# Optimization experiments

Measured on AMD Instinct MI355X. Metric: run time of the kernel, lower is better.

## Reference

```python
import jax, jax.numpy as jnp
import numpy as np

EMB = 16      # importance embedding channels (ch 0 = logit, 1: = cov features)
NSEG = 196    # n_segments (14x14 superpixel grid)
MC = 16       # num_monte_carlo
TEMP = 1.0    # initial Gumbel/RelaxedBernoulli temperature (compute_temperature(0))
JITTER = 1e-3 # numerical_stability_check: diagonal jitter so Cholesky succeeds


def setup_inputs() -> dict:
    key = jax.random.key(0)
    k1, k2, k3 = jax.random.split(key, 3)
    B, C, H, W = 16, 3, 224, 224
    x = jax.random.normal(k1, (B, C, H, W), jnp.float32)
    groups = jax.random.randint(k2, (B, H, W), 0, NSEG, jnp.int32)
    W_conv = jax.random.normal(k3, (EMB, C), jnp.float32) * 0.1
    b_conv = jnp.zeros((EMB,), jnp.float32)
    return {"x": x, "groups": groups, "W_conv": W_conv, "b_conv": b_conv}


def _group_mean(groups, emb):
    # scatter_reduce(mean, include_self=False): per-batch segment mean, 0 for empty groups
    # emb: [B,E,H,W], groups: [B,H,W] -> [B, NSEG, E]
    B, E, H, W = emb.shape
    flat = emb.reshape(B, E, H * W).transpose(0, 2, 1).reshape(B * H * W, E)
    ids = (groups.reshape(B, H * W).astype(jnp.int32)
           + NSEG * jnp.arange(B, dtype=jnp.int32)[:, None]).reshape(-1)
    sums = jax.ops.segment_sum(flat, ids, num_segments=B * NSEG).reshape(B, NSEG, E)
    cnt = jax.ops.segment_sum(jnp.ones((B * H * W,), flat.dtype), ids,
                              num_segments=B * NSEG).reshape(B, NSEG, 1)
    return sums / jnp.maximum(cnt, 1.0)


def reference(x, groups, W_conv, b_conv):
    B, C, H, W = x.shape
    # importance_predictor as 1x1 conv: [B,C,H,W] -> [B,EMB,H,W]
    emb = jnp.einsum('bchw,ec->behw', x, W_conv) + b_conv[None, :, None, None]

    avg = _group_mean(groups, emb)            # [B, NSEG, EMB]
    mu = avg[:, :, 0]                          # [B, NSEG]
    gemb = avg[:, :, 1:]                       # [B, NSEG, EMB-1]
    # groups_emb.mT @ groups_emb (groups_emb is [B, EMB-1, NSEG] in torch)
    sigma = jnp.einsum('bse,bte->bst', gemb, gemb)
    sigma = sigma + JITTER * jnp.eye(NSEG, dtype=sigma.dtype)

    pixel_probs = jax.nn.sigmoid(emb[:, 0])    # [B, H, W]
    group_probs = jax.nn.sigmoid(mu)           # [B, NSEG]

    # MultivariateNormal(mu, sigma).rsample([MC]).movedim(0,-1)
    L = jnp.linalg.cholesky(sigma)             # [B, NSEG, NSEG]
    kg, ku = jax.random.split(jax.random.key(42))
    eps = jax.random.normal(kg, (B, NSEG, MC), x.dtype)
    logits_mc = mu[:, :, None] + jnp.einsum('bst,btm->bsm', L, eps)  # [B,NSEG,MC]

    # RelaxedBernoulli(temp, probs=sigmoid(logits_mc)).rsample()
    u = jax.random.uniform(ku, (B, NSEG, MC), x.dtype, 1e-6, 1.0 - 1e-6)
    logistic = jnp.log(u) - jnp.log1p(-u)
    relaxed = jax.nn.sigmoid((logits_mc + logistic) / TEMP)
    hard = (relaxed > 0.5).astype(relaxed.dtype)
    groups_mcmc = hard + relaxed - jax.lax.stop_gradient(relaxed)  # straight-through

    # groups_to_mask: gather group decision back to every pixel
    gf = groups.reshape(B, H * W).astype(jnp.int32)
    idx = jnp.broadcast_to(gf[:, :, None], (B, H * W, MC))
    mask = jnp.take_along_axis(groups_mcmc, idx, axis=1)           # [B, HW, MC]
    mask = mask.reshape(B, H, W, MC)
    mask = jnp.broadcast_to(mask[:, None], (B, C, H, W, MC))       # expand channels
    return mask, group_probs, pixel_probs, sigma
```

## Files before the change

kernel.cpp:

```cpp
#include <hip/hip_runtime.h>
#include <stdint.h>

#define HW    50176
#define BATCH 16
#define NSEG  196
#define EMB   16
#define MC    16
#define JITTER 0.001f
#define EBLK  14
#define PXB   3584

__host__ __device__ inline void threefry2x32(uint32_t k0, uint32_t k1,
                                             uint32_t x0, uint32_t x1,
                                             uint32_t& o0, uint32_t& o1) {
  uint32_t k2 = k0 ^ k1 ^ 0x1BD11BDAu;
#define TFR(r) { x0 += x1; x1 = (x1 << (r)) | (x1 >> (32 - (r))); x1 ^= x0; }
  x0 += k0; x1 += k1;
  TFR(13) TFR(15) TFR(26) TFR(6)
  x0 += k1; x1 += k2 + 1u;
  TFR(17) TFR(29) TFR(16) TFR(24)
  x0 += k2; x1 += k0 + 2u;
  TFR(13) TFR(15) TFR(26) TFR(6)
  x0 += k0; x1 += k1 + 3u;
  TFR(17) TFR(29) TFR(16) TFR(24)
  x0 += k1; x1 += k2 + 4u;
  TFR(13) TFR(15) TFR(26) TFR(6)
  x0 += k2; x1 += k0 + 5u;
#undef TFR
  o0 = x0; o1 = x1;
}

__device__ inline float erfinv_f32(float x) {
  float w = -log1pf(-x * x);
  float p;
  if (w < 5.0f) {
    w = w - 2.5f;
    p = 2.81022636e-08f;
    p = 3.43273939e-07f + p * w;
    p = -3.5233877e-06f + p * w;
    p = -4.39150654e-06f + p * w;
    p = 0.00021858087f + p * w;
    p = -0.00125372503f + p * w;
    p = -0.00417768164f + p * w;
    p = 0.246640727f + p * w;
    p = 1.50140941f + p * w;
  } else {
    w = sqrtf(w) - 3.0f;
    p = -0.000200214257f;
    p = 0.000100950558f + p * w;
    p = 0.00134934322f + p * w;
    p = -0.00367342844f + p * w;
    p = 0.00573950773f + p * w;
    p = -0.0076224613f + p * w;
    p = 0.00943887047f + p * w;
    p = 1.00167406f + p * w;
    p = 2.83297682f + p * w;
  }
  return p * x;
}

__device__ inline float bits_to_f01(uint32_t bits) {
  uint32_t fb = (bits >> 9) | 0x3F800000u;
  return __uint_as_float(fb) - 1.0f;
}

__device__ inline float dot15(const float a[15], const float b[15]) {
  float d = 0.0f;
#pragma unroll
  for (int j = 0; j < 15; ++j) d = fmaf(a[j], b[j], d);
  return d;
}

__device__ inline void pivot_scalars(const float gk[15], float& invd,
                                     float& dd, float& beta) {
  const float sj = 0.031622776601683794f;
  float t0 = fmaf(gk[0], gk[0], JITTER);
  float t1 = gk[1] * gk[1];   float t2 = gk[2] * gk[2];
  float t3 = gk[3] * gk[3];   float t4 = gk[4] * gk[4];
  float t5 = gk[5] * gk[5];   float t6 = gk[6] * gk[6];
  float t7 = gk[7] * gk[7];   float t8 = gk[8] * gk[8];
  float t9 = gk[9] * gk[9];   float t10 = gk[10] * gk[10];
  float t11 = gk[11] * gk[11]; float t12 = gk[12] * gk[12];
  float t13 = gk[13] * gk[13]; float t14 = gk[14] * gk[14];
  float u0 = t0 + t1, u1 = t2 + t3, u2 = t4 + t5, u3 = t6 + t7;
  float u4 = t8 + t9, u5 = t10 + t11, u6 = t12 + t13;
  float v0 = u0 + u1, v1 = u2 + u3, v2 = u4 + u5, v3 = u6 + t14;
  float jn = (v0 + v1) + (v2 + v3);
  invd = __builtin_amdgcn_rsqf(jn);
  dd = jn * invd;
  beta = (invd * invd) * __builtin_amdgcn_rcpf(fmaf(sj, invd, 1.0f));
}

__global__ __launch_bounds__(256) void emb_kernel(
    const float* __restrict__ x, const int* __restrict__ groups,
    const float* __restrict__ Wc, const float* __restrict__ bc,
    float* __restrict__ partial, float* __restrict__ pixel_probs) {
  __shared__ float lsum[4 * NSEG];
  int b = blockIdx.x / EBLK;
  int blk = blockIdx.x % EBLK;
  int tid = threadIdx.x;
  for (int i = tid; i < 4 * NSEG; i += 256) lsum[i] = 0.0f;
  __syncthreads();
  const float* xb = x + (size_t)b * 3 * HW;
  float w0 = Wc[0], w1 = Wc[1], w2 = Wc[2], b0 = bc[0];
  for (int k = 0; k < PXB / 512; ++k) {
    int p = blk * PXB + (k * 256 + tid) * 2;
    float2 x0 = *(const float2*)(xb + p);
    float2 x1 = *(const float2*)(xb + HW + p);
    float2 x2 = *(const float2*)(xb + 2 * HW + p);
    int2 gg = *(const int2*)(groups + b * HW + p);
    float ea = w0 * x0.x + w1 * x1.x;
    ea = ea + w2 * x2.x + b0;
    float eb = w0 * x0.y + w1 * x1.y;
    eb = eb + w2 * x2.y + b0;
    float2 pp;
    pp.x = 1.0f / (1.0f + expf(-ea));
    pp.y = 1.0f / (1.0f + expf(-eb));
    *(float2*)(pixel_probs + b * HW + p) = pp;
    atomicAdd(&lsum[gg.x], x0.x);
    atomicAdd(&lsum[NSEG + gg.x], x1.x);
    atomicAdd(&lsum[2 * NSEG + gg.x], x2.x);
    atomicAdd(&lsum[3 * NSEG + gg.x], 1.0f);
    atomicAdd(&lsum[gg.y], x0.y);
    atomicAdd(&lsum[NSEG + gg.y], x1.y);
    atomicAdd(&lsum[2 * NSEG + gg.y], x2.y);
    atomicAdd(&lsum[3 * NSEG + gg.y], 1.0f);
  }
  __syncthreads();
  float* pb = partial + (size_t)blockIdx.x * (4 * NSEG);
  if (tid < NSEG) {
#pragma unroll
    for (int c = 0; c < 4; ++c) pb[c * NSEG + tid] = lsum[c * NSEG + tid];
  }
}

__global__ __launch_bounds__(256, 1) void main_kernel(
    const float* __restrict__ partial, const float* __restrict__ Wc,
    const float* __restrict__ bc,
    uint32_t kg0, uint32_t kg1, uint32_t ku0, uint32_t ku1,
    float* __restrict__ group_probs, float* __restrict__ sigma_out,
    float* __restrict__ hard) {
  int bid = blockIdx.x;
  int tid = threadIdx.x;

  if (bid < 112) {
    int b = bid / 7;
    int tile = bid % 7;
    __shared__ float ge_s[15][NSEG];
    if (tid < NSEG) {
      float sx0 = 0.0f, sx1 = 0.0f, sx2 = 0.0f, cn = 0.0f;
      for (int bb = 0; bb < EBLK; ++bb) {
        const float* pb = partial + (size_t)(b * EBLK + bb) * (4 * NSEG);
        sx0 += pb[tid]; sx1 += pb[NSEG + tid];
        sx2 += pb[2 * NSEG + tid]; cn += pb[3 * NSEG + tid];
      }
      float denom = fmaxf(cn, 1.0f);
#pragma unroll
      for (int j = 1; j < EMB; ++j) {
        float e = Wc[j * 3 + 0] * sx0 + Wc[j * 3 + 1] * sx1;
        e = e + Wc[j * 3 + 2] * sx2 + bc[j] * cn;
        ge_s[j - 1][tid] = e / denom;
      }
    }
    __syncthreads();
    if (tid < NSEG) {
      int t = tid;
      float gt[15];
#pragma unroll
      for (int j = 0; j < 15; ++j) gt[j] = ge_s[j][t];
      for (int r = 0; r < 28; ++r) {
        int s = tile * 28 + r;
        float a = 0.0f;
#pragma unroll
        for (int j = 0; j < 15; ++j) a = fmaf(ge_s[j][s], gt[j], a);
        if (s == t) a += JITTER;
        sigma_out[((size_t)b * NSEG + s) * NSEG + t] = a;
      }
    }
    return;
  }

  int b = bid - 112;
  __shared__ float ge[15][NSEG];
  __shared__ float mu_l[NSEG];
  __shared__ float eps_lds[NSEG * MC];
  __shared__ __align__(16) float pbuf[2][4][16];

  for (int t = tid; t < NSEG * MC; t += 256) {
    uint32_t a0, a1;
    threefry2x32(kg0, kg1, 0u, (uint32_t)(b * NSEG * MC + t), a0, a1);
    float f = bits_to_f01(a0 ^ a1);
    const float lo = -0.99999994f;
    float u = fmaxf(lo, f * (1.0f - lo) + lo);
    eps_lds[t] = 1.4142135623730951f * erfinv_f32(u);
  }

  if (tid < NSEG) {
    float sx0 = 0.0f, sx1 = 0.0f, sx2 = 0.0f, cn = 0.0f;
    for (int bb = 0; bb < EBLK; ++bb) {
      const float* pb = partial + (size_t)(b * EBLK + bb) * (4 * NSEG);
      sx0 += pb[tid]; sx1 += pb[NSEG + tid];
      sx2 += pb[2 * NSEG + tid]; cn += pb[3 * NSEG + tid];
    }
    float denom = fmaxf(cn, 1.0f);
#pragma unroll
    for (int j = 0; j < EMB; ++j) {
      float e = Wc[j * 3 + 0] * sx0 + Wc[j * 3 + 1] * sx1;
      e = e + Wc[j * 3 + 2] * sx2 + bc[j] * cn;
      float v = e / denom;
      if (j == 0) {
        mu_l[tid] = v;
        group_probs[b * NSEG + tid] = 1.0f / (1.0f + expf(-v));
      } else {
        ge[j - 1][tid] = v;
      }
    }
  }
  __syncthreads();

  int i = tid;
  float g[15];
#pragma unroll
  for (int j = 0; j < 15; ++j) g[j] = (i < NSEG) ? ge[j][i] : 0.0f;
  float acc[16];
#pragma unroll
  for (int m = 0; m < 16; ++m) acc[m] = 0.0f;
  if (tid < 4) {
    float* pw = &pbuf[0][tid][0];
#pragma unroll
    for (int j = 0; j < 15; ++j) pw[j] = g[j];
  }
  __syncthreads();

#define APPLY_PIVOT(rv, invd_, dd_, beta_, K)                               \
  {                                                                         \
    float dot = dot15(g, rv);                                               \
    float w = (i > (K)) ? dot * (invd_)                                     \
                        : ((i == (K)) ? (dd_) : 0.0f);                      \
    const float4* ep = (const float4*)(eps_lds + (K) * MC);                 \
    float4 e0 = ep[0], e1 = ep[1], e2 = ep[2], e3 = ep[3];                  \
    float ek[16] = {e0.x, e0.y, e0.z, e0.w, e1.x, e1.y, e1.z, e1.w,         \
                    e2.x, e2.y, e2.z, e2.w, e3.x, e3.y, e3.z, e3.w};        \
    _Pragma("unroll")                                                       \
    for (int m = 0; m < 16; ++m) acc[m] = fmaf(w, ek[m], acc[m]);           \
    float bd = (beta_) * dot;                                               \
    _Pragma("unroll")                                                       \
    for (int j = 0; j < 15; ++j) g[j] = fmaf(-bd, rv[j], g[j]);             \
  }

  for (int t49 = 0; t49 < 49; ++t49) {
    const float* pb0 = &pbuf[t49 & 1][0][0];
    float r0[15], r1[15], r2[15], r3[15];
    {
      float4 a0 = *(const float4*)(pb0 + 0);
      float4 a1 = *(const float4*)(pb0 + 4);
      float4 a2 = *(const float4*)(pb0 + 8);
      float4 a3 = *(const float4*)(pb0 + 12);
      r0[0]=a0.x; r0[1]=a0.y; r0[2]=a0.z; r0[3]=a0.w;
      r0[4]=a1.x; r0[5]=a1.y; r0[6]=a1.z; r0[7]=a1.w;
      r0[8]=a2.x; r0[9]=a2.y; r0[10]=a2.z; r0[11]=a2.w;
      r0[12]=a3.x; r0[13]=a3.y; r0[14]=a3.z;
      a0 = *(const float4*)(pb0 + 16); a1 = *(const float4*)(pb0 + 20);
      a2 = *(const float4*)(pb0 + 24); a3 = *(const float4*)(pb0 + 28);
      r1[0]=a0.x; r1[1]=a0.y; r1[2]=a0.z; r1[3]=a0.w;
      r1[4]=a1.x; r1[5]=a1.y; r1[6]=a1.z; r1[7]=a1.w;
      r1[8]=a2.x; r1[9]=a2.y; r1[10]=a2.z; r1[11]=a2.w;
      r1[12]=a3.x; r1[13]=a3.y; r1[14]=a3.z;
      a0 = *(const float4*)(pb0 + 32); a1 = *(const float4*)(pb0 + 36);
      a2 = *(const float4*)(pb0 + 40); a3 = *(const float4*)(pb0 + 44);
      r2[0]=a0.x; r2[1]=a0.y; r2[2]=a0.z; r2[3]=a0.w;
      r2[4]=a1.x; r2[5]=a1.y; r2[6]=a1.z; r2[7]=a1.w;
      r2[8]=a2.x; r2[9]=a2.y; r2[10]=a2.z; r2[11]=a2.w;
      r2[12]=a3.x; r2[13]=a3.y; r2[14]=a3.z;
      a0 = *(const float4*)(pb0 + 48); a1 = *(const float4*)(pb0 + 52);
      a2 = *(const float4*)(pb0 + 56); a3 = *(const float4*)(pb0 + 60);
      r3[0]=a0.x; r3[1]=a0.y; r3[2]=a0.z; r3[3]=a0.w;
      r3[4]=a1.x; r3[5]=a1.y; r3[6]=a1.z; r3[7]=a1.w;
      r3[8]=a2.x; r3[9]=a2.y; r3[10]=a2.z; r3[11]=a2.w;
      r3[12]=a3.x; r3[13]=a3.y; r3[14]=a3.z;
    }
    float invd0, dd0, beta0, invd1, dd1, beta1;
    float invd2, dd2, beta2, invd3, dd3, beta3;
    pivot_scalars(r0, invd0, dd0, beta0);
    {
      float d = dot15(r1, r0); float bd = beta0 * d;
#pragma unroll
      for (int j = 0; j < 15; ++j) r1[j] = fmaf(-bd, r0[j], r1[j]);
    }
    pivot_scalars(r1, invd1, dd1, beta1);
    {
      float d = dot15(r2, r0); float bd = beta0 * d;
#pragma unroll
      for (int j = 0; j < 15; ++j) r2[j] = fmaf(-bd, r0[j], r2[j]);
      d = dot15(r2, r1); bd = beta1 * d;
#pragma unroll
      for (int j = 0; j < 15; ++j) r2[j] = fmaf(-bd, r1[j], r2[j]);
    }
    pivot_scalars(r2, invd2, dd2, beta2);
    {
      float d = dot15(r3, r0); float bd = beta0 * d;
#pragma unroll
      for (int j = 0; j < 15; ++j) r3[j] = fmaf(-bd, r0[j], r3[j]);
      d = dot15(r3, r1); bd = beta1 * d;
#pragma unroll
      for (int j = 0; j < 15; ++j) r3[j] = fmaf(-bd, r1[j], r3[j]);
      d = dot15(r3, r2); bd = beta2 * d;
#pragma unroll
      for (int j = 0; j < 15; ++j) r3[j] = fmaf(-bd, r2[j], r3[j]);
    }
    pivot_scalars(r3, invd3, dd3, beta3);

    int k0 = 4 * t49;
    APPLY_PIVOT(r0, invd0, dd0, beta0, k0 + 0)
    APPLY_PIVOT(r1, invd1, dd1, beta1, k0 + 1)
    APPLY_PIVOT(r2, invd2, dd2, beta2, k0 + 2)
    APPLY_PIVOT(r3, invd3, dd3, beta3, k0 + 3)

    int nb = 4 * (t49 + 1);
    if (i >= nb && i < nb + 4) {
      float* pw = &pbuf[(t49 + 1) & 1][i - nb][0];
#pragma unroll
      for (int j = 0; j < 15; ++j) pw[j] = g[j];
    }
    __syncthreads();
  }
#undef APPLY_PIVOT

  if (i < NSEG) {
    float mui = mu_l[i];
    float4 outv[4];
    float* op = (float*)outv;
#pragma unroll
    for (int m = 0; m < 16; ++m) {
      uint32_t a0, a1;
      threefry2x32(ku0, ku1, 0u, (uint32_t)(b * NSEG * MC + i * MC + m), a0, a1);
      float f = bits_to_f01(a0 ^ a1);
      const float mn = 1e-6f;
      const float mx = (float)(1.0 - 1e-6);
      float uu = fmaxf(mn, f * (mx - mn) + mn);
      float lg = logf(uu) - log1pf(-uu);
      float z = mui + acc[m] + lg;
      op[m] = (z > 0.0f) ? 1.0f : 0.0f;
    }
    float4* hp = (float4*)(hard + ((size_t)b * NSEG + i) * MC);
#pragma unroll
    for (int q = 0; q < 4; ++q) hp[q] = outv[q];
  }
}

__global__ __launch_bounds__(256) void mask_kernel(
    const int* __restrict__ groups, const float* __restrict__ hard,
    float4* __restrict__ out) {
  int idx = blockIdx.x * 256 + threadIdx.x;
  if (idx >= BATCH * HW * 4) return;
  int q = idx & 3;
  int bp = idx >> 2;
  int b = bp / HW;
  int p = bp - b * HW;
  int g = groups[bp];
  float4 v = ((const float4*)hard)[(b * NSEG + g) * 4 + q];
  size_t base = ((size_t)(b * 3) * HW + p) * 4 + q;
  out[base] = v;
  out[base + (size_t)HW * 4] = v;
  out[base + (size_t)2 * HW * 4] = v;
}

extern "C" void kernel_launch(void* const* d_in, const int* in_sizes, int n_in,
                              void* d_out, int out_size, void* d_ws, size_t ws_size,
                              hipStream_t stream) {
  const float* x = (const float*)d_in[0];
  const int* groups = (const int*)d_in[1];
  const float* Wc = (const float*)d_in[2];
  const float* bc = (const float*)d_in[3];

  float* out = (float*)d_out;
  float* mask_out = out;
  float* gp_out = out + 38535168;
  float* pp_out = gp_out + 3136;
  float* sig_out = pp_out + 802816;

  float* ws = (float*)d_ws;
  float* partial = ws;
  float* hard    = ws + 175616;

  emb_kernel<<<BATCH * EBLK, 256, 0, stream>>>(x, groups, Wc, bc, partial, pp_out);

  uint32_t kg0, kg1, ku0, ku1;
  threefry2x32(0u, 42u, 0u, 0u, kg0, kg1);
  threefry2x32(0u, 42u, 0u, 1u, ku0, ku1);

  main_kernel<<<128, 256, 0, stream>>>(partial, Wc, bc, kg0, kg1, ku0, ku1,
                                       gp_out, sig_out, hard);
  mask_kernel<<<(BATCH * HW * 4 + 255) / 256, 256, 0, stream>>>(
      groups, hard, (float4*)mask_out);
}
```

Before: 254.1 us.

## Run Cholesky sampling in a single wavefront with readlane broadcasts; use nontemporal stores

The low-rank Cholesky/sampling loop moves from a 256-thread block synchronised with LDS double-buffering and __syncthreads to a single 64-lane wavefront. Each lane holds four rows, and pivot rows are broadcast with readlane, so block barriers and LDS pivot traffic go away. The mask and pixel_probs outputs now use nontemporal stores to cut cache pollution on the large streaming writes. The trade-off is that each lane now does four times the per-pivot work serially, with higher register pressure and one wave per block.

```diff
diff --git a/kernel.cpp b/kernel.cpp
--- a/kernel.cpp
+++ b/kernel.cpp
@@ -9,6 +9,9 @@
 #define JITTER 0.001f
 #define EBLK  14
 #define PXB   3584
+
+typedef float f32x2 __attribute__((ext_vector_type(2)));
+typedef float f32x4 __attribute__((ext_vector_type(4)));
 
 __host__ __device__ inline void threefry2x32(uint32_t k0, uint32_t k1,
                                              uint32_t x0, uint32_t x1,
@@ -91,6 +94,10 @@
   beta = (invd * invd) * __builtin_amdgcn_rcpf(fmaf(sj, invd, 1.0f));
 }
 
+__device__ inline float bcast_lane(float v, int lane) {
+  return __uint_as_float(__builtin_amdgcn_readlane(__float_as_uint(v), lane));
+}
+
 __global__ __launch_bounds__(256) void emb_kernel(
     const float* __restrict__ x, const int* __restrict__ groups,
     const float* __restrict__ Wc, const float* __restrict__ bc,
@@ -113,10 +120,10 @@
     ea = ea + w2 * x2.x + b0;
     float eb = w0 * x0.y + w1 * x1.y;
     eb = eb + w2 * x2.y + b0;
-    float2 pp;
+    f32x2 pp;
     pp.x = 1.0f / (1.0f + expf(-ea));
     pp.y = 1.0f / (1.0f + expf(-eb));
-    *(float2*)(pixel_probs + b * HW + p) = pp;
+    __builtin_nontemporal_store(pp, (f32x2*)(pixel_probs + b * HW + p));
     atomicAdd(&lsum[gg.x], x0.x);
     atomicAdd(&lsum[NSEG + gg.x], x1.x);
     atomicAdd(&lsum[2 * NSEG + gg.x], x2.x);
@@ -184,7 +191,6 @@
   __shared__ float ge[15][NSEG];
   __shared__ float mu_l[NSEG];
   __shared__ float eps_lds[NSEG * MC];
-  __shared__ __align__(16) float pbuf[2][4][16];
 
   for (int t = tid; t < NSEG * MC; t += 256) {
     uint32_t a0, a1;
@@ -218,139 +224,89 @@
   }
   __syncthreads();
 
-  int i = tid;
-  float g[15];
-#pragma unroll
-  for (int j = 0; j < 15; ++j) g[j] = (i < NSEG) ? ge[j][i] : 0.0f;
-  float acc[16];
-#pragma unroll
-  for (int m = 0; m < 16; ++m) acc[m] = 0.0f;
-  if (tid < 4) {
-    float* pw = &pbuf[0][tid][0];
-#pragma unroll
-    for (int j = 0; j < 15; ++j) pw[j] = g[j];
-  }
-  __syncthreads();
-
-#define APPLY_PIVOT(rv, invd_, dd_, beta_, K)                               \
+  if (tid >= 64) return;
+  int lane = tid;
+
+  float g0[15], g1[15], g2[15], g3[15];
+#pragma unroll
+  for (int j = 0; j < 15; ++j) {
+    g0[j] = ge[j][lane];
+    g1[j] = ge[j][64 + lane];
+    g2[j] = ge[j][128 + lane];
+    g3[j] = (192 + lane < NSEG) ? ge[j][192 + lane] : 0.0f;
+  }
+  float ac0[16], ac1[16], ac2[16], ac3[16];
+#pragma unroll
+  for (int m = 0; m < 16; ++m) { ac0[m] = 0.0f; ac1[m] = 0.0f; ac2[m] = 0.0f; ac3[m] = 0.0f; }
+
+#define SLOT(gs, accs, S)                                                   \
   {                                                                         \
-    float dot = dot15(g, rv);                                               \
-    float w = (i > (K)) ? dot * (invd_)                                     \
-                        : ((i == (K)) ? (dd_) : 0.0f);                      \
-    const float4* ep = (const float4*)(eps_lds + (K) * MC);                 \
-    float4 e0 = ep[0], e1 = ep[1], e2 = ep[2], e3 = ep[3];                  \
+    float dot = dot15(gs, rv);                                              \
+    int r = (S) * 64 + lane;                                                \
+    float w = (r > k) ? dot * invd : ((r == k) ? dd : 0.0f);                \
+    _Pragma("unroll")                                                       \
+    for (int m = 0; m < 16; ++m) accs[m] = fmaf(w, ek[m], accs[m]);         \
+    float bd = beta * dot;                                                  \
+    _Pragma("unroll")                                                       \
+    for (int j = 0; j < 15; ++j) gs[j] = fmaf(-bd, rv[j], gs[j]);           \
+  }
+
+#define CHOL_PIVOT(GP, LOFF, BODY)                                          \
+  {                                                                         \
+    float rv[15];                                                           \
+    _Pragma("unroll")                                                       \
+    for (int j = 0; j < 15; ++j) rv[j] = bcast_lane(GP[j], k - (LOFF));     \
+    float invd, dd, beta;                                                   \
+    pivot_scalars(rv, invd, dd, beta);                                      \
+    const f32x4* ep4 = (const f32x4*)(eps_lds + k * MC);                    \
+    f32x4 e0 = ep4[0], e1 = ep4[1], e2 = ep4[2], e3 = ep4[3];               \
     float ek[16] = {e0.x, e0.y, e0.z, e0.w, e1.x, e1.y, e1.z, e1.w,         \
                     e2.x, e2.y, e2.z, e2.w, e3.x, e3.y, e3.z, e3.w};        \
-    _Pragma("unroll")                                                       \
-    for (int m = 0; m < 16; ++m) acc[m] = fmaf(w, ek[m], acc[m]);           \
-    float bd = (beta_) * dot;                                               \
-    _Pragma("unroll")                                                       \
-    for (int j = 0; j < 15; ++j) g[j] = fmaf(-bd, rv[j], g[j]);             \
-  }
-
-  for (int t49 = 0; t49 < 49; ++t49) {
-    const float* pb0 = &pbuf[t49 & 1][0][0];
-    float r0[15], r1[15], r2[15], r3[15];
-    {
-      float4 a0 = *(const float4*)(pb0 + 0);
-      float4 a1 = *(const float4*)(pb0 + 4);
-      float4 a2 = *(const float4*)(pb0 + 8);
-      float4 a3 = *(const float4*)(pb0 + 12);
-      r0[0]=a0.x; r0[1]=a0.y; r0[2]=a0.z; r0[3]=a0.w;
-      r0[4]=a1.x; r0[5]=a1.y; r0[6]=a1.z; r0[7]=a1.w;
-      r0[8]=a2.x; r0[9]=a2.y; r0[10]=a2.z; r0[11]=a2.w;
-      r0[12]=a3.x; r0[13]=a3.y; r0[14]=a3.z;
-      a0 = *(const float4*)(pb0 + 16); a1 = *(const float4*)(pb0 + 20);
-      a2 = *(const float4*)(pb0 + 24); a3 = *(const float4*)(pb0 + 28);
-      r1[0]=a0.x; r1[1]=a0.y; r1[2]=a0.z; r1[3]=a0.w;
-      r1[4]=a1.x; r1[5]=a1.y; r1[6]=a1.z; r1[7]=a1.w;
-      r1[8]=a2.x; r1[9]=a2.y; r1[10]=a2.z; r1[11]=a2.w;
-      r1[12]=a3.x; r1[13]=a3.y; r1[14]=a3.z;
-      a0 = *(const float4*)(pb0 + 32); a1 = *(const float4*)(pb0 + 36);
-      a2 = *(const float4*)(pb0 + 40); a3 = *(const float4*)(pb0 + 44);
-      r2[0]=a0.x; r2[1]=a0.y; r2[2]=a0.z; r2[3]=a0.w;
-      r2[4]=a1.x; r2[5]=a1.y; r2[6]=a1.z; r2[7]=a1.w;
-      r2[8]=a2.x; r2[9]=a2.y; r2[10]=a2.z; r2[11]=a2.w;
-      r2[12]=a3.x; r2[13]=a3.y; r2[14]=a3.z;
-      a0 = *(const float4*)(pb0 + 48); a1 = *(const float4*)(pb0 + 52);
-      a2 = *(const float4*)(pb0 + 56); a3 = *(const float4*)(pb0 + 60);
-      r3[0]=a0.x; r3[1]=a0.y; r3[2]=a0.z; r3[3]=a0.w;
-      r3[4]=a1.x; r3[5]=a1.y; r3[6]=a1.z; r3[7]=a1.w;
-      r3[8]=a2.x; r3[9]=a2.y; r3[10]=a2.z; r3[11]=a2.w;
-      r3[12]=a3.x; r3[13]=a3.y; r3[14]=a3.z;
-    }
-    float invd0, dd0, beta0, invd1, dd1, beta1;
-    float invd2, dd2, beta2, invd3, dd3, beta3;
-    pivot_scalars(r0, invd0, dd0, beta0);
-    {
-      float d = dot15(r1, r0); float bd = beta0 * d;
-#pragma unroll
-      for (int j = 0; j < 15; ++j) r1[j] = fmaf(-bd, r0[j], r1[j]);
-    }
-    pivot_scalars(r1, invd1, dd1, beta1);
-    {
-      float d = dot15(r2, r0); float bd = beta0 * d;
-#pragma unroll
-      for (int j = 0; j < 15; ++j) r2[j] = fmaf(-bd, r0[j], r2[j]);
-      d = dot15(r2, r1); bd = beta1 * d;
-#pragma unroll
-      for (int j = 0; j < 15; ++j) r2[j] = fmaf(-bd, r1[j], r2[j]);
-    }
-    pivot_scalars(r2, invd2, dd2, beta2);
-    {
-      float d = dot15(r3, r0); float bd = beta0 * d;
-#pragma unroll
-      for (int j = 0; j < 15; ++j) r3[j] = fmaf(-bd, r0[j], r3[j]);
-      d = dot15(r3, r1); bd = beta1 * d;
-#pragma unroll
-      for (int j = 0; j < 15; ++j) r3[j] = fmaf(-bd, r1[j], r3[j]);
-      d = dot15(r3, r2); bd = beta2 * d;
-#pragma unroll
-      for (int j = 0; j < 15; ++j) r3[j] = fmaf(-bd, r2[j], r3[j]);
-    }
-    pivot_scalars(r3, invd3, dd3, beta3);
-
-    int k0 = 4 * t49;
-    APPLY_PIVOT(r0, invd0, dd0, beta0, k0 + 0)
-    APPLY_PIVOT(r1, invd1, dd1, beta1, k0 + 1)
-    APPLY_PIVOT(r2, invd2, dd2, beta2, k0 + 2)
-    APPLY_PIVOT(r3, invd3, dd3, beta3, k0 + 3)
-
-    int nb = 4 * (t49 + 1);
-    if (i >= nb && i < nb + 4) {
-      float* pw = &pbuf[(t49 + 1) & 1][i - nb][0];
-#pragma unroll
-      for (int j = 0; j < 15; ++j) pw[j] = g[j];
-    }
-    __syncthreads();
-  }
-#undef APPLY_PIVOT
-
-  if (i < NSEG) {
-    float mui = mu_l[i];
-    float4 outv[4];
-    float* op = (float*)outv;
-#pragma unroll
-    for (int m = 0; m < 16; ++m) {
-      uint32_t a0, a1;
-      threefry2x32(ku0, ku1, 0u, (uint32_t)(b * NSEG * MC + i * MC + m), a0, a1);
-      float f = bits_to_f01(a0 ^ a1);
-      const float mn = 1e-6f;
-      const float mx = (float)(1.0 - 1e-6);
-      float uu = fmaxf(mn, f * (mx - mn) + mn);
-      float lg = logf(uu) - log1pf(-uu);
-      float z = mui + acc[m] + lg;
-      op[m] = (z > 0.0f) ? 1.0f : 0.0f;
-    }
-    float4* hp = (float4*)(hard + ((size_t)b * NSEG + i) * MC);
-#pragma unroll
-    for (int q = 0; q < 4; ++q) hp[q] = outv[q];
-  }
+    BODY                                                                    \
+  }
+
+  for (int k = 0; k < 64; ++k)
+    CHOL_PIVOT(g0, 0, SLOT(g0, ac0, 0) SLOT(g1, ac1, 1) SLOT(g2, ac2, 2) SLOT(g3, ac3, 3))
+  for (int k = 64; k < 128; ++k)
+    CHOL_PIVOT(g1, 64, SLOT(g1, ac1, 1) SLOT(g2, ac2, 2) SLOT(g3, ac3, 3))
+  for (int k = 128; k < 192; ++k)
+    CHOL_PIVOT(g2, 128, SLOT(g2, ac2, 2) SLOT(g3, ac3, 3))
+  for (int k = 192; k < 196; ++k)
+    CHOL_PIVOT(g3, 192, SLOT(g3, ac3, 3))
+#undef CHOL_PIVOT
+#undef SLOT
+
+#define EPI(accs, S)                                                        \
+  {                                                                         \
+    int r = (S) * 64 + lane;                                                \
+    if (r < NSEG) {                                                         \
+      float mui = mu_l[r];                                                  \
+      f32x4 outv[4];                                                        \
+      float* op = (float*)outv;                                             \
+      _Pragma("unroll")                                                     \
+      for (int m = 0; m < 16; ++m) {                                        \
+        uint32_t a0, a1;                                                    \
+        threefry2x32(ku0, ku1, 0u,                                          \
+                     (uint32_t)(b * NSEG * MC + r * MC + m), a0, a1);       \
+        float f = bits_to_f01(a0 ^ a1);                                     \
+        const float mn = 1e-6f;                                             \
+        const float mx = (float)(1.0 - 1e-6);                               \
+        float uu = fmaxf(mn, f * (mx - mn) + mn);                           \
+        float lg = logf(uu) - log1pf(-uu);                                  \
+        float z = mui + accs[m] + lg;                                       \
+        op[m] = (z > 0.0f) ? 1.0f : 0.0f;                                   \
+      }                                                                     \
+      f32x4* hp = (f32x4*)(hard + ((size_t)b * NSEG + r) * MC);             \
+      hp[0] = outv[0]; hp[1] = outv[1]; hp[2] = outv[2]; hp[3] = outv[3];   \
+    }                                                                       \
+  }
+  EPI(ac0, 0) EPI(ac1, 1) EPI(ac2, 2) EPI(ac3, 3)
+#undef EPI
 }
 
 __global__ __launch_bounds__(256) void mask_kernel(
     const int* __restrict__ groups, const float* __restrict__ hard,
-    float4* __restrict__ out) {
+    f32x4* __restrict__ out) {
   int idx = blockIdx.x * 256 + threadIdx.x;
   if (idx >= BATCH * HW * 4) return;
   int q = idx & 3;
@@ -358,11 +314,11 @@
   int b = bp / HW;
   int p = bp - b * HW;
   int g = groups[bp];
-  float4 v = ((const float4*)hard)[(b * NSEG + g) * 4 + q];
+  f32x4 v = ((const f32x4*)hard)[(b * NSEG + g) * 4 + q];
   size_t base = ((size_t)(b * 3) * HW + p) * 4 + q;
-  out[base] = v;
-  out[base + (size_t)HW * 4] = v;
-  out[base + (size_t)2 * HW * 4] = v;
+  __builtin_nontemporal_store(v, &out[base]);
+  __builtin_nontemporal_store(v, &out[base + (size_t)HW * 4]);
+  __builtin_nontemporal_store(v, &out[base + (size_t)2 * HW * 4]);
 }
 
 extern "C" void kernel_launch(void* const* d_in, const int* in_sizes, int n_in,
@@ -392,5 +348,5 @@
   main_kernel<<<128, 256, 0, stream>>>(partial, Wc, bc, kg0, kg1, ku0, ku1,
                                        gp_out, sig_out, hard);
   mask_kernel<<<(BATCH * HW * 4 + 255) / 256, 256, 0, stream>>>(
-      groups, hard, (float4*)mask_out);
-}
+      groups, hard, (f32x4*)mask_out);
+}
```

Measured after the change: 451.6 us. 1.78x slower.

## Pack two independent work items per 512-thread block in main kernel

Applied to the files above, without the earlier changes.

Merges pairs of 256-thread work units (sigma tiles or per-batch Cholesky/sampling) into a single 512-thread block with split shared memory, halving the grid from 128 to 64 blocks. The intent is to cut block count and scheduling overhead, and to place two latency-bound serial Cholesky chains on one CU so they hide each other's latency. The cost is that __syncthreads now makes both halves wait on each other, and each block uses more shared memory and registers.

```diff
diff --git a/kernel.cpp b/kernel.cpp
--- a/kernel.cpp
+++ b/kernel.cpp
@@ -9,6 +9,15 @@
 #define JITTER 0.001f
 #define EBLK  14
 #define PXB   3584
+
+#define SL_GE   0
+#define SL_MU   2940
+#define SL_EPS  3136
+#define SL_PBUF 6272
+#define SL_SIZE 6400
+
+typedef float f32x2  __attribute__((ext_vector_type(2)));
+typedef float f32x4  __attribute__((ext_vector_type(4)));
 
 __host__ __device__ inline void threefry2x32(uint32_t k0, uint32_t k1,
                                              uint32_t x0, uint32_t x1,
@@ -134,7 +143,7 @@
   }
 }
 
-__global__ __launch_bounds__(256, 1) void main_kernel(
+__global__ __launch_bounds__(512, 1) void main_kernel(
     const float* __restrict__ partial, const float* __restrict__ Wc,
     const float* __restrict__ bc,
     uint32_t kg0, uint32_t kg1, uint32_t ku0, uint32_t ku1,
@@ -142,37 +151,44 @@
     float* __restrict__ hard) {
   int bid = blockIdx.x;
   int tid = threadIdx.x;
-
-  if (bid < 112) {
-    int b = bid / 7;
-    int tile = bid % 7;
-    __shared__ float ge_s[15][NSEG];
-    if (tid < NSEG) {
+  int inst = tid >> 8;
+  int t = tid & 255;
+
+  __shared__ __align__(16) float smem[2 * SL_SIZE];
+  float* ge   = smem + inst * SL_SIZE + SL_GE;
+  float* mu_l = smem + inst * SL_SIZE + SL_MU;
+  float* eps  = smem + inst * SL_SIZE + SL_EPS;
+  float* pbuf = smem + inst * SL_SIZE + SL_PBUF;
+
+  if (bid < 56) {
+    int T = bid * 2 + inst;
+    int b = T / 7;
+    int tile = T % 7;
+    if (t < NSEG) {
       float sx0 = 0.0f, sx1 = 0.0f, sx2 = 0.0f, cn = 0.0f;
       for (int bb = 0; bb < EBLK; ++bb) {
         const float* pb = partial + (size_t)(b * EBLK + bb) * (4 * NSEG);
-        sx0 += pb[tid]; sx1 += pb[NSEG + tid];
-        sx2 += pb[2 * NSEG + tid]; cn += pb[3 * NSEG + tid];
+        sx0 += pb[t]; sx1 += pb[NSEG + t];
+        sx2 += pb[2 * NSEG + t]; cn += pb[3 * NSEG + t];
       }
       float denom = fmaxf(cn, 1.0f);
 #pragma unroll
       for (int j = 1; j < EMB; ++j) {
         float e = Wc[j * 3 + 0] * sx0 + Wc[j * 3 + 1] * sx1;
         e = e + Wc[j * 3 + 2] * sx2 + bc[j] * cn;
-        ge_s[j - 1][tid] = e / denom;
+        ge[(j - 1) * NSEG + t] = e / denom;
       }
     }
     __syncthreads();
-    if (tid < NSEG) {
-      int t = tid;
+    if (t < NSEG) {
       float gt[15];
 #pragma unroll
-      for (int j = 0; j < 15; ++j) gt[j] = ge_s[j][t];
+      for (int j = 0; j < 15; ++j) gt[j] = ge[j * NSEG + t];
       for (int r = 0; r < 28; ++r) {
         int s = tile * 28 + r;
         float a = 0.0f;
 #pragma unroll
-        for (int j = 0; j < 15; ++j) a = fmaf(ge_s[j][s], gt[j], a);
+        for (int j = 0; j < 15; ++j) a = fmaf(ge[j * NSEG + s], gt[j], a);
         if (s == t) a += JITTER;
         sigma_out[((size_t)b * NSEG + s) * NSEG + t] = a;
       }
@@ -180,27 +196,23 @@
     return;
   }
 
-  int b = bid - 112;
-  __shared__ float ge[15][NSEG];
-  __shared__ float mu_l[NSEG];
-  __shared__ float eps_lds[NSEG * MC];
-  __shared__ __align__(16) float pbuf[2][4][16];
-
-  for (int t = tid; t < NSEG * MC; t += 256) {
+  int b = (bid - 56) * 2 + inst;
+
+  for (int e = t; e < NSEG * MC; e += 256) {
     uint32_t a0, a1;
-    threefry2x32(kg0, kg1, 0u, (uint32_t)(b * NSEG * MC + t), a0, a1);
+    threefry2x32(kg0, kg1, 0u, (uint32_t)(b * NSEG * MC + e), a0, a1);
     float f = bits_to_f01(a0 ^ a1);
     const float lo = -0.99999994f;
     float u = fmaxf(lo, f * (1.0f - lo) + lo);
-    eps_lds[t] = 1.4142135623730951f * erfinv_f32(u);
-  }
-
-  if (tid < NSEG) {
+    eps[e] = 1.4142135623730951f * erfinv_f32(u);
+  }
+
+  if (t < NSEG) {
     float sx0 = 0.0f, sx1 = 0.0f, sx2 = 0.0f, cn = 0.0f;
     for (int bb = 0; bb < EBLK; ++bb) {
       const float* pb = partial + (size_t)(b * EBLK + bb) * (4 * NSEG);
-      sx0 += pb[tid]; sx1 += pb[NSEG + tid];
-      sx2 += pb[2 * NSEG + tid]; cn += pb[3 * NSEG + tid];
+      sx0 += pb[t]; sx1 += pb[NSEG + t];
+      sx2 += pb[2 * NSEG + t]; cn += pb[3 * NSEG + t];
     }
     float denom = fmaxf(cn, 1.0f);
 #pragma unroll
@@ -209,24 +221,24 @@
       e = e + Wc[j * 3 + 2] * sx2 + bc[j] * cn;
       float v = e / denom;
       if (j == 0) {
-        mu_l[tid] = v;
-        group_probs[b * NSEG + tid] = 1.0f / (1.0f + expf(-v));
+        mu_l[t] = v;
+        group_probs[b * NSEG + t] = 1.0f / (1.0f + expf(-v));
       } else {
-        ge[j - 1][tid] = v;
+        ge[(j - 1) * NSEG + t] = v;
       }
     }
   }
   __syncthreads();
 
-  int i = tid;
+  int i = t;
   float g[15];
 #pragma unroll
-  for (int j = 0; j < 15; ++j) g[j] = (i < NSEG) ? ge[j][i] : 0.0f;
+  for (int j = 0; j < 15; ++j) g[j] = (i < NSEG) ? ge[j * NSEG + i] : 0.0f;
   float acc[16];
 #pragma unroll
   for (int m = 0; m < 16; ++m) acc[m] = 0.0f;
-  if (tid < 4) {
-    float* pw = &pbuf[0][tid][0];
+  if (t < 4) {
+    float* pw = pbuf + t * 16;
 #pragma unroll
     for (int j = 0; j < 15; ++j) pw[j] = g[j];
   }
@@ -237,7 +249,7 @@
     float dot = dot15(g, rv);                                               \
     float w = (i > (K)) ? dot * (invd_)                                     \
                         : ((i == (K)) ? (dd_) : 0.0f);                      \
-    const float4* ep = (const float4*)(eps_lds + (K) * MC);                 \
+    const float4* ep = (const float4*)(eps + (K) * MC);                     \
     float4 e0 = ep[0], e1 = ep[1], e2 = ep[2], e3 = ep[3];                  \
     float ek[16] = {e0.x, e0.y, e0.z, e0.w, e1.x, e1.y, e1.z, e1.w,         \
                     e2.x, e2.y, e2.z, e2.w, e3.x, e3.y, e3.z, e3.w};        \
@@ -249,7 +261,7 @@
   }
 
   for (int t49 = 0; t49 < 49; ++t49) {
-    const float* pb0 = &pbuf[t49 & 1][0][0];
+    const float* pb0 = pbuf + (t49 & 1) * 64;
     float r0[15], r1[15], r2[15], r3[15];
     {
       float4 a0 = *(const float4*)(pb0 + 0);
@@ -318,7 +330,7 @@
 
     int nb = 4 * (t49 + 1);
     if (i >= nb && i < nb + 4) {
-      float* pw = &pbuf[(t49 + 1) & 1][i - nb][0];
+      float* pw = pbuf + ((t49 + 1) & 1) * 64 + (i - nb) * 16;
 #pragma unroll
       for (int j = 0; j < 15; ++j) pw[j] = g[j];
     }
@@ -389,8 +401,8 @@
   threefry2x32(0u, 42u, 0u, 0u, kg0, kg1);
   threefry2x32(0u, 42u, 0u, 1u, ku0, ku1);
 
-  main_kernel<<<128, 256, 0, stream>>>(partial, Wc, bc, kg0, kg1, ku0, ku1,
-                                       gp_out, sig_out, hard);
+  main_kernel<<<64, 512, 0, stream>>>(partial, Wc, bc, kg0, kg1, ku0, ku1,
+                                      gp_out, sig_out, hard);
   mask_kernel<<<(BATCH * HW * 4 + 255) / 256, 256, 0, stream>>>(
       groups, hard, (float4*)mask_out);
 }
```

After: 291.2 us. 14.6% more time.
